# Optimization experiments

Hardware: AMD Instinct MI355X
Metric: run time of the kernel (lower is better)

Reference implementation:

```python
import jax, jax.numpy as jnp
import numpy as np

L = 4          # num_levels
N = 32768      # memory slots per level
D_S, D_E, D_C, D_K, D_V, D_Z = 1024, 1024, 512, 128, 512, 128
THR = 0.1      # sparse_write_threshold
EPS = 1e-5


def setup_inputs() -> dict:
    key = jax.random.key(0)
    ks = jax.random.split(key, 16)
    w = lambda k, shape, s=0.02: jax.random.normal(k, shape, dtype=jnp.float32) * s
    return {
        "s_t": jax.random.normal(ks[0], (D_S,), dtype=jnp.float32),
        "e_t": jax.random.normal(ks[1], (D_E,), dtype=jnp.float32),
        "level_contexts": jax.random.normal(ks[2], (L, D_C), dtype=jnp.float32),
        "M": jax.random.normal(ks[3], (L, N, D_V), dtype=jnp.float32) * 0.1,
        "K_mem": jax.random.normal(ks[4], (L, N, D_K), dtype=jnp.float32) * 0.1,
        "decay": jnp.full((L,), 0.01, dtype=jnp.float32),
        "W1_0": w(ks[5], (D_Z, D_S + D_E)),
        "b1_0": jnp.zeros((D_Z,), jnp.float32),
        "W1_r": w(ks[6], (L - 1, D_Z, D_S + D_C + D_E)),
        "b1_r": jnp.zeros((L - 1, D_Z), jnp.float32),
        "spec_wr": w(ks[7], (L, 1, D_Z), 1.0),
        "spec_wi": w(ks[8], (L, 1, D_Z), 1.0),
        "ln_g": jnp.ones((L, D_Z), jnp.float32),
        "ln_b": jnp.zeros((L, D_Z), jnp.float32),
        "Wg": w(ks[9], (L, 1, D_Z), 0.5),
        "bg": jnp.zeros((L, 1), jnp.float32),
        "Wv": w(ks[10], (L, D_V, D_Z)),
        "bv": jnp.zeros((L, D_V), jnp.float32),
        "Wk": w(ks[11], (L, D_K, D_Z)),
        "bk": jnp.zeros((L, D_K), jnp.float32),
    }


def _level_update(ell, x, M, K_mem, decay, W1, b1, spec_wr, spec_wi,
                  ln_g, ln_b, Wg, bg, Wv, bv, Wk, bk):
    # Linear -> SpectralBlock (seq_len=1 FFT filter) -> LayerNorm
    h = W1 @ x + b1                                  # [d_z]
    X = jnp.fft.rfft(h[None, :], axis=0)             # [1, d_z] complex
    Y = X * (spec_wr[ell] + 1j * spec_wi[ell])       # learned spectral filter
    y = jnp.fft.irfft(Y, n=1, axis=0)[0]             # [d_z]
    mu = y.mean()
    var = ((y - mu) ** 2).mean()
    z = (y - mu) * jax.lax.rsqrt(var + EPS) * ln_g[ell] + ln_b[ell]

    g = jax.nn.sigmoid(Wg[ell] @ z + bg[ell])[0]     # scalar write gate
    v = jnp.tanh(Wv[ell] @ z + bv[ell])              # [d_v]
    k = Wk[ell] @ z + bk[ell]                        # [d_k]

    scores = (K_mem[ell] @ k) / np.sqrt(D_K).astype(np.float32)  # [N]
    alpha = jax.nn.softmax(scores)                   # [N]

    # sparse-write branch: if g < threshold, no write (pure decay)
    wgt = jnp.where(g >= THR, g, jnp.float32(0.0))
    keep = (1.0 - decay[ell])
    M_new = keep * M[ell] + wgt * alpha[:, None] * v[None, :]      # [N, d_v]
    K_new = keep * K_mem[ell] + wgt * alpha[:, None] * k[None, :]  # [N, d_k]
    return jnp.concatenate([M_new, K_new], axis=-1)  # [N, d_v + d_k]


def reference(s_t, e_t, level_contexts, M, K_mem, decay, W1_0, b1_0, W1_r, b1_r,
              spec_wr, spec_wi, ln_g, ln_b, Wg, bg, Wv, bv, Wk, bk):
    outs = []
    for ell in range(L):
        if ell == 0:
            x = jnp.concatenate([s_t, e_t])
            W1, b1 = W1_0, b1_0
        else:
            x = jnp.concatenate([s_t, level_contexts[ell - 1], e_t])
            W1, b1 = W1_r[ell - 1], b1_r[ell - 1]
        outs.append(_level_update(ell, x, M, K_mem, decay, W1, b1, spec_wr,
                                  spec_wi, ln_g, ln_b, Wg, bg, Wv, bv, Wk, bk))
    return jnp.stack(outs)  # [L, N, d_v + d_k]
```

## Files before the change

kernel.cpp:

```cpp
#include <hip/hip_runtime.h>
#include <hip/hip_bf16.h>
#include <math.h>

#define NLVL 4
#define NSLOT 32768
#define SB 128

typedef float f4 __attribute__((ext_vector_type(4)));

__global__ __launch_bounds__(256) void k_h(
    const float* __restrict__ s_t, const float* __restrict__ e_t,
    const float* __restrict__ ctx,
    const float* __restrict__ W1_0, const float* __restrict__ b1_0,
    const float* __restrict__ W1_r, const float* __restrict__ b1_r,
    const float* __restrict__ spec_wr, float* __restrict__ ybuf)
{
    const int row = blockIdx.x;
    const int ell = blockIdx.y;
    const int tid = threadIdx.x;
    const int d = (ell == 0) ? 2048 : 2560;
    const float* W1 = (ell == 0) ? W1_0 : (W1_r + (size_t)(ell - 1) * 128 * 2560);
    const float* b1 = (ell == 0) ? b1_0 : (b1_r + (ell - 1) * 128);
    const f4* wrow = (const f4*)(W1 + (size_t)row * d);

    float acc = 0.f;
    if (ell == 0) {
        for (int i4 = tid; i4 < 512; i4 += 256) {
            f4 w = wrow[i4];
            f4 x = (i4 < 256) ? ((const f4*)s_t)[i4]
                              : ((const f4*)e_t)[i4 - 256];
            acc += w.x * x.x + w.y * x.y + w.z * x.z + w.w * x.w;
        }
    } else {
        const f4* c4 = (const f4*)(ctx + (size_t)(ell - 1) * 512);
        for (int i4 = tid; i4 < 640; i4 += 256) {
            f4 w = wrow[i4];
            f4 x;
            if (i4 < 256)      x = ((const f4*)s_t)[i4];
            else if (i4 < 384) x = c4[i4 - 256];
            else               x = ((const f4*)e_t)[i4 - 384];
            acc += w.x * x.x + w.y * x.y + w.z * x.z + w.w * x.w;
        }
    }
    __shared__ float red[256];
    red[tid] = acc;
    __syncthreads();
    for (int off = 128; off > 0; off >>= 1) {
        if (tid < off) red[tid] += red[tid + off];
        __syncthreads();
    }
    if (tid == 0)
        ybuf[ell * 128 + row] = (red[0] + b1[row]) * spec_wr[ell * 128 + row];
}

__global__ __launch_bounds__(128) void k_z(
    const float* __restrict__ ybuf,
    const float* __restrict__ ln_g, const float* __restrict__ ln_b,
    const float* __restrict__ Wg, const float* __restrict__ bg,
    const float* __restrict__ decay,
    float* __restrict__ zbuf, float* __restrict__ wgt, float* __restrict__ keepb)
{
    const int ell = blockIdx.x;
    const int t = threadIdx.x;
    __shared__ float red[128];
    float y = ybuf[ell * 128 + t];
    red[t] = y;
    __syncthreads();
    for (int off = 64; off > 0; off >>= 1) {
        if (t < off) red[t] += red[t + off];
        __syncthreads();
    }
    float mu = red[0] * (1.f / 128.f);
    __syncthreads();
    float dd = y - mu;
    red[t] = dd * dd;
    __syncthreads();
    for (int off = 64; off > 0; off >>= 1) {
        if (t < off) red[t] += red[t + off];
        __syncthreads();
    }
    float rstd = rsqrtf(red[0] * (1.f / 128.f) + 1e-5f);
    float z = dd * rstd * ln_g[ell * 128 + t] + ln_b[ell * 128 + t];
    zbuf[ell * 128 + t] = z;
    __syncthreads();
    red[t] = Wg[ell * 128 + t] * z;
    __syncthreads();
    for (int off = 64; off > 0; off >>= 1) {
        if (t < off) red[t] += red[t + off];
        __syncthreads();
    }
    if (t == 0) {
        float g = 1.f / (1.f + expf(-(red[0] + bg[ell])));
        wgt[ell] = (g >= 0.1f) ? g : 0.f;
        keepb[ell] = 1.f - decay[ell];
    }
}

__global__ __launch_bounds__(256) void k_vk(
    const float* __restrict__ zbuf,
    const float* __restrict__ Wv, const float* __restrict__ bv,
    const float* __restrict__ Wk, const float* __restrict__ bk,
    float* __restrict__ vvec, float* __restrict__ kvec)
{
    const int ell = blockIdx.y;
    const int tid = threadIdx.x;
    __shared__ float sz[128];
    if (tid < 128) sz[tid] = zbuf[ell * 128 + tid];
    __syncthreads();

    const int r = blockIdx.x * 64 + (tid >> 2);
    const int lane = tid & 3;
    const float* wrow;
    float bias;
    float* outp;
    bool is_v = (r < 512);
    if (is_v) {
        wrow = Wv + ((size_t)ell * 512 + r) * 128;
        bias = bv[ell * 512 + r];
        outp = vvec + ell * 512 + r;
    } else {
        int rk = r - 512;
        wrow = Wk + ((size_t)ell * 128 + rk) * 128;
        bias = bk[ell * 128 + rk];
        outp = kvec + ell * 128 + rk;
    }
    float a = 0.f;
    const f4* w4 = (const f4*)wrow + lane * 8;
    const float* z0 = sz + lane * 32;
    #pragma unroll
    for (int j = 0; j < 8; ++j) {
        f4 w = w4[j];
        a += w.x * z0[j * 4] + w.y * z0[j * 4 + 1] + w.z * z0[j * 4 + 2] + w.w * z0[j * 4 + 3];
    }
    a += __shfl_xor(a, 1);
    a += __shfl_xor(a, 2);
    if (lane == 0) {
        float val = a + bias;
        if (is_v) val = tanhf(val);
        *outp = val;
    }
}

__global__ __launch_bounds__(256) void k_scores(
    const float* __restrict__ K_mem, const float* __restrict__ kvec,
    float* __restrict__ expsc, float* __restrict__ partial)
{
    const int ell = blockIdx.y;
    const int tid = threadIdx.x;
    __shared__ float sk[128];
    __shared__ float red[256];
    if (tid < 128) sk[tid] = kvec[ell * 128 + tid];
    __syncthreads();

    const int n0 = blockIdx.x * (NSLOT / SB);
    const int gid = tid >> 4, lane = tid & 15;
    const float* z0 = sk + lane * 8;
    const float scale = 0.08838834764831845f;
    float acc = 0.f;
    for (int it = 0; it < 16; ++it) {
        int n = n0 + it * 16 + gid;
        const f4* kr = (const f4*)(K_mem + ((size_t)ell * NSLOT + n) * 128) + lane * 2;
        f4 wa = kr[0], wb = kr[1];
        float a = wa.x * z0[0] + wa.y * z0[1] + wa.z * z0[2] + wa.w * z0[3]
                + wb.x * z0[4] + wb.y * z0[5] + wb.z * z0[6] + wb.w * z0[7];
        #pragma unroll
        for (int m = 1; m < 16; m <<= 1) a += __shfl_xor(a, m);
        if (lane == 0) {
            float e = expf(a * scale);
            expsc[(size_t)ell * NSLOT + n] = e;
            acc += e;
        }
    }
    red[tid] = acc;
    __syncthreads();
    for (int off = 128; off > 0; off >>= 1) {
        if (tid < off) red[tid] += red[tid + off];
        __syncthreads();
    }
    if (tid == 0) partial[ell * SB + blockIdx.x] = red[0];
}

__global__ __launch_bounds__(256) void k_write(
    const float* __restrict__ M, const float* __restrict__ K_mem,
    const float* __restrict__ expsc, const float* __restrict__ partial,
    const float* __restrict__ wgt, const float* __restrict__ keepb,
    const float* __restrict__ vvec, const float* __restrict__ kvec,
    f4* __restrict__ out)
{
    __shared__ f4 sv4[512];
    __shared__ f4 sk4[128];
    __shared__ float sp[512];
    __shared__ float sscl[4], skeep[4];
    const int tid = threadIdx.x;
    for (int i = tid; i < 512; i += 256) {
        sv4[i] = ((const f4*)vvec)[i];
        sp[i] = partial[i];
    }
    for (int i = tid; i < 128; i += 256) sk4[i] = ((const f4*)kvec)[i];
    __syncthreads();
    if (tid < 4) {
        float s = 0.f;
        for (int j = 0; j < SB; ++j) s += sp[tid * SB + j];
        sscl[tid] = wgt[tid] / s;
        skeep[tid] = keepb[tid];
    }
    __syncthreads();

    const int total = NLVL * NSLOT * 160;
    const int stride = gridDim.x * blockDim.x;
    for (int idx = blockIdx.x * blockDim.x + tid; idx < total; idx += stride) {
        int row = idx / 160;
        int j4 = idx - row * 160;
        int ell = row >> 15;
        float c = expsc[row] * sscl[ell];
        float keep = skeep[ell];
        f4 o;
        if (j4 < 128) {
            f4 m = __builtin_nontemporal_load((const f4*)M + (size_t)row * 128 + j4);
            f4 vv = sv4[(ell << 7) + j4];
            o.x = keep * m.x + c * vv.x;
            o.y = keep * m.y + c * vv.y;
            o.z = keep * m.z + c * vv.z;
            o.w = keep * m.w + c * vv.w;
        } else {
            int jk = j4 - 128;
            f4 kk = __builtin_nontemporal_load((const f4*)K_mem + (size_t)row * 32 + jk);
            f4 kv = sk4[(ell << 5) + jk];
            o.x = keep * kk.x + c * kv.x;
            o.y = keep * kk.y + c * kv.y;
            o.z = keep * kk.z + c * kv.z;
            o.w = keep * kk.w + c * kv.w;
        }
        __builtin_nontemporal_store(o, out + idx);
    }
}

extern "C" void kernel_launch(void* const* d_in, const int* in_sizes, int n_in,
                              void* d_out, int out_size, void* d_ws, size_t ws_size,
                              hipStream_t stream) {
    const float* s_t    = (const float*)d_in[0];
    const float* e_t    = (const float*)d_in[1];
    const float* ctx    = (const float*)d_in[2];
    const float* M      = (const float*)d_in[3];
    const float* K_mem  = (const float*)d_in[4];
    const float* decay  = (const float*)d_in[5];
    const float* W1_0   = (const float*)d_in[6];
    const float* b1_0   = (const float*)d_in[7];
    const float* W1_r   = (const float*)d_in[8];
    const float* b1_r   = (const float*)d_in[9];
    const float* spec_wr= (const float*)d_in[10];
    const float* ln_g   = (const float*)d_in[12];
    const float* ln_b   = (const float*)d_in[13];
    const float* Wg     = (const float*)d_in[14];
    const float* bg     = (const float*)d_in[15];
    const float* Wv     = (const float*)d_in[16];
    const float* bv     = (const float*)d_in[17];
    const float* Wk     = (const float*)d_in[18];
    const float* bk     = (const float*)d_in[19];

    float* ws = (float*)d_ws;
    float* expsc   = ws;
    float* partial = ws + 131072;
    float* ybuf    = ws + 131584;
    float* zbuf    = ws + 132096;
    float* kvec    = ws + 132608;
    float* vvec    = ws + 133120;
    float* wgt     = ws + 135168;
    float* keepb   = ws + 135172;

    dim3 gh(128, NLVL);
    k_h<<<gh, 256, 0, stream>>>(s_t, e_t, ctx, W1_0, b1_0, W1_r, b1_r,
                                spec_wr, ybuf);

    k_z<<<NLVL, 128, 0, stream>>>(ybuf, ln_g, ln_b, Wg, bg, decay,
                                  zbuf, wgt, keepb);

    dim3 gvk(10, NLVL);
    k_vk<<<gvk, 256, 0, stream>>>(zbuf, Wv, bv, Wk, bk, vvec, kvec);

    dim3 gs(SB, NLVL);
    k_scores<<<gs, 256, 0, stream>>>(K_mem, kvec, expsc, partial);

    k_write<<<2048, 256, 0, stream>>>(M, K_mem, expsc, partial, wgt, keepb,
                                      vvec, kvec, (f4*)d_out);
}
```

Measured before the change: 150.9 us.

## Fuse scores and write into cooperative kernel with grid sync; merge z and vk

Merges the layernorm/gate kernel with the v/k projection kernel, with each block recomputing the layernorm. Replaces the separate scores and write kernels with one cooperative kernel of 1024 blocks. Each block scores its 128 rows into shared memory, grid-syncs to exchange per-level softmax partial sums, then writes the output rows while its K_mem tile is likely still in cache. This removes the global exp-score buffer, two launches and a second pass over K_mem, at the cost of a grid-wide barrier and a co-residency requirement of 4 blocks per CU.

```diff
diff --git a/kernel.cpp b/kernel.cpp
--- a/kernel.cpp
+++ b/kernel.cpp
@@ -1,10 +1,12 @@
 #include <hip/hip_runtime.h>
 #include <hip/hip_bf16.h>
+#include <hip/hip_cooperative_groups.h>
 #include <math.h>
+
+namespace cg = cooperative_groups;
 
 #define NLVL 4
 #define NSLOT 32768
-#define SB 128
 
 typedef float f4 __attribute__((ext_vector_type(4)));
 
@@ -53,18 +55,23 @@
         ybuf[ell * 128 + row] = (red[0] + b1[row]) * spec_wr[ell * 128 + row];
 }
 
-__global__ __launch_bounds__(128) void k_z(
+__global__ __launch_bounds__(256) void k_zvk(
     const float* __restrict__ ybuf,
     const float* __restrict__ ln_g, const float* __restrict__ ln_b,
     const float* __restrict__ Wg, const float* __restrict__ bg,
     const float* __restrict__ decay,
-    float* __restrict__ zbuf, float* __restrict__ wgt, float* __restrict__ keepb)
+    const float* __restrict__ Wv, const float* __restrict__ bv,
+    const float* __restrict__ Wk, const float* __restrict__ bk,
+    float* __restrict__ vvec, float* __restrict__ kvec,
+    float* __restrict__ wgt, float* __restrict__ keepb)
 {
-    const int ell = blockIdx.x;
+    const int ell = blockIdx.y;
     const int t = threadIdx.x;
     __shared__ float red[128];
-    float y = ybuf[ell * 128 + t];
-    red[t] = y;
+    __shared__ float sz[128];
+
+    float y = 0.f;
+    if (t < 128) { y = ybuf[ell * 128 + t]; red[t] = y; }
     __syncthreads();
     for (int off = 64; off > 0; off >>= 1) {
         if (t < off) red[t] += red[t + off];
@@ -73,43 +80,30 @@
     float mu = red[0] * (1.f / 128.f);
     __syncthreads();
     float dd = y - mu;
-    red[t] = dd * dd;
+    if (t < 128) red[t] = dd * dd;
     __syncthreads();
     for (int off = 64; off > 0; off >>= 1) {
         if (t < off) red[t] += red[t + off];
         __syncthreads();
     }
     float rstd = rsqrtf(red[0] * (1.f / 128.f) + 1e-5f);
-    float z = dd * rstd * ln_g[ell * 128 + t] + ln_b[ell * 128 + t];
-    zbuf[ell * 128 + t] = z;
-    __syncthreads();
-    red[t] = Wg[ell * 128 + t] * z;
+    __syncthreads();
+    if (t < 128) sz[t] = dd * rstd * ln_g[ell * 128 + t] + ln_b[ell * 128 + t];
+    __syncthreads();
+    if (t < 128) red[t] = Wg[ell * 128 + t] * sz[t];
     __syncthreads();
     for (int off = 64; off > 0; off >>= 1) {
         if (t < off) red[t] += red[t + off];
         __syncthreads();
     }
-    if (t == 0) {
+    if (t == 0 && blockIdx.x == 0) {
         float g = 1.f / (1.f + expf(-(red[0] + bg[ell])));
         wgt[ell] = (g >= 0.1f) ? g : 0.f;
         keepb[ell] = 1.f - decay[ell];
     }
-}
-
-__global__ __launch_bounds__(256) void k_vk(
-    const float* __restrict__ zbuf,
-    const float* __restrict__ Wv, const float* __restrict__ bv,
-    const float* __restrict__ Wk, const float* __restrict__ bk,
-    float* __restrict__ vvec, float* __restrict__ kvec)
-{
-    const int ell = blockIdx.y;
-    const int tid = threadIdx.x;
-    __shared__ float sz[128];
-    if (tid < 128) sz[tid] = zbuf[ell * 128 + tid];
-    __syncthreads();
-
-    const int r = blockIdx.x * 64 + (tid >> 2);
-    const int lane = tid & 3;
+
+    const int r = blockIdx.x * 64 + (t >> 2);
+    const int lane = t & 3;
     const float* wrow;
     float bias;
     float* outp;
@@ -141,25 +135,38 @@
     }
 }
 
-__global__ __launch_bounds__(256) void k_scores(
-    const float* __restrict__ K_mem, const float* __restrict__ kvec,
-    float* __restrict__ expsc, float* __restrict__ partial)
+__global__ __launch_bounds__(256, 4) void k_fused(
+    const float* __restrict__ M, const float* __restrict__ K_mem,
+    const float* __restrict__ kvec, const float* __restrict__ vvec,
+    const float* __restrict__ wgt, const float* __restrict__ keepb,
+    float* __restrict__ partial, f4* __restrict__ out)
 {
-    const int ell = blockIdx.y;
+    const int b = blockIdx.x;
     const int tid = threadIdx.x;
+    const int ell = b >> 8;
+    const int r0 = b << 7;
+
     __shared__ float sk[128];
+    __shared__ float se[128];
     __shared__ float red[256];
-    if (tid < 128) sk[tid] = kvec[ell * 128 + tid];
-    __syncthreads();
-
-    const int n0 = blockIdx.x * (NSLOT / SB);
+    __shared__ f4 sv4[128];
+    __shared__ f4 skv4[32];
+
+    if (tid < 128) {
+        sk[tid] = kvec[ell * 128 + tid];
+        sv4[tid] = ((const f4*)vvec)[ell * 128 + tid];
+    } else if (tid < 160) {
+        skv4[tid - 128] = ((const f4*)kvec)[ell * 32 + (tid - 128)];
+    }
+    __syncthreads();
+
     const int gid = tid >> 4, lane = tid & 15;
     const float* z0 = sk + lane * 8;
     const float scale = 0.08838834764831845f;
     float acc = 0.f;
-    for (int it = 0; it < 16; ++it) {
-        int n = n0 + it * 16 + gid;
-        const f4* kr = (const f4*)(K_mem + ((size_t)ell * NSLOT + n) * 128) + lane * 2;
+    for (int it = 0; it < 8; ++it) {
+        int rl = it * 16 + gid;
+        const f4* kr = (const f4*)K_mem + ((size_t)(r0 + rl)) * 32 + lane * 2;
         f4 wa = kr[0], wb = kr[1];
         float a = wa.x * z0[0] + wa.y * z0[1] + wa.z * z0[2] + wa.w * z0[3]
                 + wb.x * z0[4] + wb.y * z0[5] + wb.z * z0[6] + wb.w * z0[7];
@@ -167,7 +174,7 @@
         for (int m = 1; m < 16; m <<= 1) a += __shfl_xor(a, m);
         if (lane == 0) {
             float e = expf(a * scale);
-            expsc[(size_t)ell * NSLOT + n] = e;
+            se[rl] = e;
             acc += e;
         }
     }
@@ -177,61 +184,56 @@
         if (tid < off) red[tid] += red[tid + off];
         __syncthreads();
     }
-    if (tid == 0) partial[ell * SB + blockIdx.x] = red[0];
-}
-
-__global__ __launch_bounds__(256) void k_write(
-    const float* __restrict__ M, const float* __restrict__ K_mem,
-    const float* __restrict__ expsc, const float* __restrict__ partial,
-    const float* __restrict__ wgt, const float* __restrict__ keepb,
-    const float* __restrict__ vvec, const float* __restrict__ kvec,
-    f4* __restrict__ out)
-{
-    __shared__ f4 sv4[512];
-    __shared__ f4 sk4[128];
-    __shared__ float sp[512];
-    __shared__ float sscl[4], skeep[4];
-    const int tid = threadIdx.x;
-    for (int i = tid; i < 512; i += 256) {
-        sv4[i] = ((const f4*)vvec)[i];
-        sp[i] = partial[i];
-    }
-    for (int i = tid; i < 128; i += 256) sk4[i] = ((const f4*)kvec)[i];
-    __syncthreads();
-    if (tid < 4) {
-        float s = 0.f;
-        for (int j = 0; j < SB; ++j) s += sp[tid * SB + j];
-        sscl[tid] = wgt[tid] / s;
-        skeep[tid] = keepb[tid];
-    }
-    __syncthreads();
-
-    const int total = NLVL * NSLOT * 160;
-    const int stride = gridDim.x * blockDim.x;
-    for (int idx = blockIdx.x * blockDim.x + tid; idx < total; idx += stride) {
-        int row = idx / 160;
-        int j4 = idx - row * 160;
-        int ell = row >> 15;
-        float c = expsc[row] * sscl[ell];
-        float keep = skeep[ell];
-        f4 o;
-        if (j4 < 128) {
-            f4 m = __builtin_nontemporal_load((const f4*)M + (size_t)row * 128 + j4);
-            f4 vv = sv4[(ell << 7) + j4];
-            o.x = keep * m.x + c * vv.x;
-            o.y = keep * m.y + c * vv.y;
-            o.z = keep * m.z + c * vv.z;
-            o.w = keep * m.w + c * vv.w;
-        } else {
-            int jk = j4 - 128;
-            f4 kk = __builtin_nontemporal_load((const f4*)K_mem + (size_t)row * 32 + jk);
-            f4 kv = sk4[(ell << 5) + jk];
-            o.x = keep * kk.x + c * kv.x;
-            o.y = keep * kk.y + c * kv.y;
-            o.z = keep * kk.z + c * kv.z;
-            o.w = keep * kk.w + c * kv.w;
-        }
-        __builtin_nontemporal_store(o, out + idx);
+    if (tid == 0) partial[b] = red[0];
+
+    cg::this_grid().sync();
+
+    float p = partial[(ell << 8) + tid];
+    red[tid] = p;
+    __syncthreads();
+    for (int off = 128; off > 0; off >>= 1) {
+        if (tid < off) red[tid] += red[tid + off];
+        __syncthreads();
+    }
+    const float scl = wgt[ell] / red[0];
+    const float keep = keepb[ell];
+
+    int dr[5], dj[5];
+    #pragma unroll
+    for (int k2 = 0; k2 < 5; ++k2) {
+        int pos = tid + k2 * 256;
+        dr[k2] = pos / 160;
+        dj[k2] = pos - dr[k2] * 160;
+    }
+
+    const size_t ob = (size_t)r0 * 160;
+    for (int mi = 0; mi < 16; ++mi) {
+        const int rowb = mi * 8;
+        #pragma unroll
+        for (int k2 = 0; k2 < 5; ++k2) {
+            int rl = rowb + dr[k2];
+            int j4 = dj[k2];
+            float c = se[rl] * scl;
+            size_t grow = (size_t)(r0 + rl);
+            f4 o;
+            if (j4 < 128) {
+                f4 m = __builtin_nontemporal_load((const f4*)M + grow * 128 + j4);
+                f4 vv = sv4[j4];
+                o.x = keep * m.x + c * vv.x;
+                o.y = keep * m.y + c * vv.y;
+                o.z = keep * m.z + c * vv.z;
+                o.w = keep * m.w + c * vv.w;
+            } else {
+                int jk = j4 - 128;
+                f4 kk = ((const f4*)K_mem)[grow * 32 + jk];
+                f4 kv = skv4[jk];
+                o.x = keep * kk.x + c * kv.x;
+                o.y = keep * kk.y + c * kv.y;
+                o.z = keep * kk.z + c * kv.z;
+                o.w = keep * kk.w + c * kv.w;
+            }
+            __builtin_nontemporal_store(o, out + ob + (size_t)mi * 1280 + tid + k2 * 256);
+        }
     }
 }
 
@@ -259,28 +261,24 @@
     const float* bk     = (const float*)d_in[19];
 
     float* ws = (float*)d_ws;
-    float* expsc   = ws;
-    float* partial = ws + 131072;
-    float* ybuf    = ws + 131584;
-    float* zbuf    = ws + 132096;
-    float* kvec    = ws + 132608;
-    float* vvec    = ws + 133120;
-    float* wgt     = ws + 135168;
-    float* keepb   = ws + 135172;
+    float* partial = ws;
+    float* ybuf    = ws + 1024;
+    float* kvec    = ws + 1536;
+    float* vvec    = ws + 2048;
+    float* wgt     = ws + 4096;
+    float* keepb   = ws + 4100;
 
     dim3 gh(128, NLVL);
     k_h<<<gh, 256, 0, stream>>>(s_t, e_t, ctx, W1_0, b1_0, W1_r, b1_r,
                                 spec_wr, ybuf);
 
-    k_z<<<NLVL, 128, 0, stream>>>(ybuf, ln_g, ln_b, Wg, bg, decay,
-                                  zbuf, wgt, keepb);
-
-    dim3 gvk(10, NLVL);
-    k_vk<<<gvk, 256, 0, stream>>>(zbuf, Wv, bv, Wk, bk, vvec, kvec);
-
-    dim3 gs(SB, NLVL);
-    k_scores<<<gs, 256, 0, stream>>>(K_mem, kvec, expsc, partial);
-
-    k_write<<<2048, 256, 0, stream>>>(M, K_mem, expsc, partial, wgt, keepb,
-                                      vvec, kvec, (f4*)d_out);
-}
+    dim3 gzvk(10, NLVL);
+    k_zvk<<<gzvk, 256, 0, stream>>>(ybuf, ln_g, ln_b, Wg, bg, decay,
+                                    Wv, bv, Wk, bk, vvec, kvec, wgt, keepb);
+
+    f4* outp = (f4*)d_out;
+    void* args[] = {(void*)&M, (void*)&K_mem, (void*)&kvec, (void*)&vvec,
+                    (void*)&wgt, (void*)&keepb, (void*)&partial, (void*)&outp};
+    hipLaunchCooperativeKernel((void*)k_fused, dim3(1024), dim3(256),
+                               args, 0, stream);
+}
```

After: 197.7 us. +31.0%, slower.
